# Optimization experiments

Measured on AMD Instinct MI355X. Metric: run time of the kernel, lower is better.

## Reference

```python
import jax, jax.numpy as jnp
import numpy as np

R = 16
LORA_ALPHA = 16.0
SCALING = LORA_ALPHA / R  # = 1.0, matches lora_alpha / r


def setup_inputs() -> dict:
    key = jax.random.key(0)
    k_x, k_a, k_a0, k_b = jax.random.split(key, 4)
    d, r, n_tok = 4096, R, 8192
    inv_sqrt_d = 1.0 / np.sqrt(d)
    x = jax.random.normal(k_x, (n_tok, d), dtype=jnp.float32)
    # mode='standard': A0 ~ N(0, 1/d), B0 = 0; A, B initialized as clones of A0, B0
    A0 = jax.random.normal(k_a0, (r, d), dtype=jnp.float32) * inv_sqrt_d
    B0 = jnp.zeros((d, r), dtype=jnp.float32)
    # perturb A, B slightly to emulate trained params (still faithful math)
    A = A0 + jax.random.normal(k_a, (r, d), dtype=jnp.float32) * inv_sqrt_d
    B = B0 + jax.random.normal(k_b, (d, r), dtype=jnp.float32) * inv_sqrt_d
    return {"x": x, "A": A, "B": B, "A0": A0, "B0": B0}


def reference(x, A, B, A0, B0):
    # Faithful to torch: dW = (B @ A - B0 @ A0) * scaling; out = x @ dW
    # (mode='standard' uses the offset-subtracted delta)
    dW = (B @ A - B0 @ A0) * SCALING          # [d, d]
    return x @ dW                              # [N, d]
```

## Files before the change

kernel.cpp:

```cpp
#include <hip/hip_runtime.h>

#define N_TOK 8192
#define D     4096
#define RLO   16
#define R2    32

typedef __bf16  bf16x8  __attribute__((ext_vector_type(8)));
typedef short   short8v __attribute__((ext_vector_type(8)));
typedef float   f32x4   __attribute__((ext_vector_type(4)));

__device__ __forceinline__ short bf1(float f) {
  __bf16 b = (__bf16)f;
  return __builtin_bit_cast(short, b);
}

__device__ __forceinline__ short8v cvt8(float4 lo, float4 hi) {
  bf16x8 b;
  b[0] = (__bf16)lo.x; b[1] = (__bf16)lo.y; b[2] = (__bf16)lo.z; b[3] = (__bf16)lo.w;
  b[4] = (__bf16)hi.x; b[5] = (__bf16)hi.y; b[6] = (__bf16)hi.z; b[7] = (__bf16)hi.w;
  return __builtin_bit_cast(short8v, b);
}


__global__ __launch_bounds__(256) void prep_kernel(
    const float* __restrict__ A, const float* __restrict__ B,
    const float* __restrict__ A0, const float* __restrict__ B0,
    ushort* __restrict__ PTb, ushort* __restrict__ Qpk) {
  int idx = blockIdx.x * 256 + threadIdx.x;
  int r = idx >> 12;
  int k = idx & (D - 1);
  float pt, q;
  if (r < RLO) {
    pt = B[k * RLO + r];
    q  = A[r * D + k];
  } else {
    pt = -B0[k * RLO + (r - RLO)];
    q  = A0[(r - RLO) * D + k];
  }
  PTb[idx] = (ushort)bf1(pt);
  Qpk[(size_t)k * R2 + r] = (ushort)bf1(q);
}

__global__ __launch_bounds__(256) void s1_kernel(
    const float* __restrict__ x, const ushort* __restrict__ PTb,
    float* __restrict__ u) {
  __shared__ float red[4][16][R2 + 2];
  const int tid  = threadIdx.x;
  const int w    = tid >> 6;
  const int lane = tid & 63;
  const int l16  = lane & 15;
  const int kg   = lane >> 4;
  const int row0 = blockIdx.x * 16;
  const int kb   = w * 1024 + kg * 8;

  const float*  xp = x   + (size_t)(row0 + l16) * D + kb;
  const ushort* pb0 = PTb + (size_t)l16 * D + kb;
  const ushort* pb1 = pb0 + (size_t)16 * D;

  f32x4 acc0 = {0.f, 0.f, 0.f, 0.f};
  f32x4 acc1 = {0.f, 0.f, 0.f, 0.f};

#pragma unroll
  for (int s = 0; s < 32; ++s) {
    const int ko = s * 32;
    const float4 alo = *(const float4*)(xp + ko);
    const float4 ahi = *(const float4*)(xp + ko + 4);
    const short8v b0 = *(const short8v*)(pb0 + ko);
    const short8v b1 = *(const short8v*)(pb1 + ko);
    const short8v a  = cvt8(alo, ahi);
    acc0 = __builtin_amdgcn_mfma_f32_16x16x32_bf16(a, b0, acc0, 0, 0, 0);
    acc1 = __builtin_amdgcn_mfma_f32_16x16x32_bf16(a, b1, acc1, 0, 0, 0);
  }

#pragma unroll
  for (int j = 0; j < 4; ++j) {
    red[w][kg * 4 + j][l16]      = acc0[j];
    red[w][kg * 4 + j][16 + l16] = acc1[j];
  }
  __syncthreads();

#pragma unroll
  for (int half = 0; half < 2; ++half) {
    const int idx = half * 256 + tid;
    const int row = idx >> 5;
    const int r   = idx & 31;
    const float s = red[0][row][r] + red[1][row][r] +
                    red[2][row][r] + red[3][row][r];
    u[(size_t)(row0 + row) * R2 + r] = s;
  }
}

__global__ __launch_bounds__(256) void s2_kernel(
    const float* __restrict__ u, const ushort* __restrict__ Qpk,
    float* __restrict__ out) {
  __shared__ __align__(16) ushort usb[32][R2];
  const int tid = threadIdx.x;
  const int rowblk = (int)blockIdx.x >> 2;
  const int jseg   = blockIdx.x & 3;
  const int row0 = rowblk * 32;

  {
    const int row = tid >> 3;
    const int r4  = (tid & 7) * 4;
    const float4 v = *(const float4*)(u + (size_t)(row0 + row) * R2 + r4);
    usb[row][r4 + 0] = (ushort)bf1(v.x);
    usb[row][r4 + 1] = (ushort)bf1(v.y);
    usb[row][r4 + 2] = (ushort)bf1(v.z);
    usb[row][r4 + 3] = (ushort)bf1(v.w);
  }
  __syncthreads();

  const int w    = tid >> 6;
  const int lane = tid & 63;
  const int l16  = lane & 15;
  const int kg   = lane >> 4;
  const int jbase = jseg * 1024 + w * 256;

  const short8v ua0 = *(const short8v*)&usb[l16][kg * 8];
  const short8v ua1 = *(const short8v*)&usb[16 + l16][kg * 8];
  const f32x4 z = {0.f, 0.f, 0.f, 0.f};

#pragma unroll
  for (int jt = 0; jt < 16; ++jt) {
    const int j = jbase + jt * 16 + l16;
    const short8v qb = *(const short8v*)(Qpk + (size_t)j * R2 + kg * 8);
    const f32x4 d0 = __builtin_amdgcn_mfma_f32_16x16x32_bf16(ua0, qb, z, 0, 0, 0);
    const f32x4 d1 = __builtin_amdgcn_mfma_f32_16x16x32_bf16(ua1, qb, z, 0, 0, 0);
    float* o = out + (size_t)(row0 + kg * 4) * D + j;
#pragma unroll
    for (int jr = 0; jr < 4; ++jr) {
      o[(size_t)jr * D]        = d0[jr];
      o[(size_t)(16 + jr) * D] = d1[jr];
    }
  }
}

extern "C" void kernel_launch(void* const* d_in, const int* in_sizes, int n_in,
                              void* d_out, int out_size, void* d_ws, size_t ws_size,
                              hipStream_t stream) {
  const float* x  = (const float*)d_in[0];
  const float* A  = (const float*)d_in[1];
  const float* B  = (const float*)d_in[2];
  const float* A0 = (const float*)d_in[3];
  const float* B0 = (const float*)d_in[4];
  float* out = (float*)d_out;

  ushort* PTb = (ushort*)d_ws;
  ushort* Qpk = PTb + (size_t)R2 * D;
  float*  u   = (float*)(Qpk + (size_t)D * R2);

  hipLaunchKernelGGL(prep_kernel, dim3((R2 * D) / 256), dim3(256), 0, stream,
                     A, B, A0, B0, PTb, Qpk);
  hipLaunchKernelGGL(s1_kernel, dim3(N_TOK / 16), dim3(256), 0, stream,
                     x, PTb, u);
  hipLaunchKernelGGL(s2_kernel, dim3((N_TOK / 32) * 4), dim3(256), 0, stream,
                     u, Qpk, out);
}
```

Before: 66.68 us.

## Fuse low-rank projection and expansion stages into a single kernel

Merges the x·Pᵀ reduction kernel and the u·Q expansion kernel into one kernel. The intermediate u is kept in shared memory as bf16 instead of going through global memory, and one kernel launch is dropped. Each block now writes a 16-row slab of the full 4096-wide output, and the stores switch to nontemporal hints. In exchange each block does a long serial store phase after the reduction, and the loads of x can no longer overlap with the output writes across separate kernels.

Result: faster. 64.38 us (-3.4%).

```diff
diff --git a/kernel.cpp b/kernel.cpp
--- a/kernel.cpp
+++ b/kernel.cpp
@@ -41,10 +41,11 @@
   Qpk[(size_t)k * R2 + r] = (ushort)bf1(q);
 }
 
-__global__ __launch_bounds__(256) void s1_kernel(
+__global__ __launch_bounds__(256) void fused_kernel(
     const float* __restrict__ x, const ushort* __restrict__ PTb,
-    float* __restrict__ u) {
+    const ushort* __restrict__ Qpk, float* __restrict__ out) {
   __shared__ float red[4][16][R2 + 2];
+  __shared__ __align__(16) ushort usb[16][R2];
   const int tid  = threadIdx.x;
   const int w    = tid >> 6;
   const int lane = tid & 63;
@@ -53,7 +54,7 @@
   const int row0 = blockIdx.x * 16;
   const int kb   = w * 1024 + kg * 8;
 
-  const float*  xp = x   + (size_t)(row0 + l16) * D + kb;
+  const float*  xp  = x   + (size_t)(row0 + l16) * D + kb;
   const ushort* pb0 = PTb + (size_t)l16 * D + kb;
   const ushort* pb1 = pb0 + (size_t)16 * D;
 
@@ -86,52 +87,23 @@
     const int r   = idx & 31;
     const float s = red[0][row][r] + red[1][row][r] +
                     red[2][row][r] + red[3][row][r];
-    u[(size_t)(row0 + row) * R2 + r] = s;
-  }
-}
-
-__global__ __launch_bounds__(256) void s2_kernel(
-    const float* __restrict__ u, const ushort* __restrict__ Qpk,
-    float* __restrict__ out) {
-  __shared__ __align__(16) ushort usb[32][R2];
-  const int tid = threadIdx.x;
-  const int rowblk = (int)blockIdx.x >> 2;
-  const int jseg   = blockIdx.x & 3;
-  const int row0 = rowblk * 32;
-
-  {
-    const int row = tid >> 3;
-    const int r4  = (tid & 7) * 4;
-    const float4 v = *(const float4*)(u + (size_t)(row0 + row) * R2 + r4);
-    usb[row][r4 + 0] = (ushort)bf1(v.x);
-    usb[row][r4 + 1] = (ushort)bf1(v.y);
-    usb[row][r4 + 2] = (ushort)bf1(v.z);
-    usb[row][r4 + 3] = (ushort)bf1(v.w);
+    usb[row][r] = (ushort)bf1(s);
   }
   __syncthreads();
 
-  const int w    = tid >> 6;
-  const int lane = tid & 63;
-  const int l16  = lane & 15;
-  const int kg   = lane >> 4;
-  const int jbase = jseg * 1024 + w * 256;
+  const short8v ua = *(const short8v*)&usb[l16][kg * 8];
+  const f32x4 z = {0.f, 0.f, 0.f, 0.f};
+  const int jbase = w * 1024;
 
-  const short8v ua0 = *(const short8v*)&usb[l16][kg * 8];
-  const short8v ua1 = *(const short8v*)&usb[16 + l16][kg * 8];
-  const f32x4 z = {0.f, 0.f, 0.f, 0.f};
-
-#pragma unroll
-  for (int jt = 0; jt < 16; ++jt) {
+#pragma unroll 8
+  for (int jt = 0; jt < 64; ++jt) {
     const int j = jbase + jt * 16 + l16;
     const short8v qb = *(const short8v*)(Qpk + (size_t)j * R2 + kg * 8);
-    const f32x4 d0 = __builtin_amdgcn_mfma_f32_16x16x32_bf16(ua0, qb, z, 0, 0, 0);
-    const f32x4 d1 = __builtin_amdgcn_mfma_f32_16x16x32_bf16(ua1, qb, z, 0, 0, 0);
+    const f32x4 d = __builtin_amdgcn_mfma_f32_16x16x32_bf16(ua, qb, z, 0, 0, 0);
     float* o = out + (size_t)(row0 + kg * 4) * D + j;
 #pragma unroll
-    for (int jr = 0; jr < 4; ++jr) {
-      o[(size_t)jr * D]        = d0[jr];
-      o[(size_t)(16 + jr) * D] = d1[jr];
-    }
+    for (int jr = 0; jr < 4; ++jr)
+      __builtin_nontemporal_store(d[jr], o + (size_t)jr * D);
   }
 }
 
@@ -147,12 +119,9 @@
 
   ushort* PTb = (ushort*)d_ws;
   ushort* Qpk = PTb + (size_t)R2 * D;
-  float*  u   = (float*)(Qpk + (size_t)D * R2);
 
   hipLaunchKernelGGL(prep_kernel, dim3((R2 * D) / 256), dim3(256), 0, stream,
                      A, B, A0, B0, PTb, Qpk);
-  hipLaunchKernelGGL(s1_kernel, dim3(N_TOK / 16), dim3(256), 0, stream,
-                     x, PTb, u);
-  hipLaunchKernelGGL(s2_kernel, dim3((N_TOK / 32) * 4), dim3(256), 0, stream,
-                     u, Qpk, out);
+  hipLaunchKernelGGL(fused_kernel, dim3(N_TOK / 16), dim3(256), 0, stream,
+                     x, PTb, Qpk, out);
 }
```
